# Kernel tuning notes

Measured on AMD Instinct MI355X. Metric: run time of the kernel, lower is better.

## Reference

```python
import jax, jax.numpy as jnp
import numpy as np

IN_CH = 512
STYLE_DIM = 512
K_ATT = 4  # block size used in forward()


def make_up_kernel():
    # make_kernel([1,3,3,1]) -> outer product, normalized; Upsample scales by factor**2
    k = jnp.array([1.0, 3.0, 3.0, 1.0], jnp.float32)
    k = k[None, :] * k[:, None]
    k = k / k.sum()
    return k * 4.0  # factor**2 with factor=2


def setup_inputs() -> dict:
    key = jax.random.key(0)
    ks = jax.random.split(key, 8)
    B, H, W = 8, 128, 128
    return {
        "input": jax.random.normal(ks[0], (B, IN_CH, H, W), jnp.float32),
        "style": jax.random.normal(ks[1], (B, STYLE_DIM), jnp.float32),
        "skip": jax.random.normal(ks[2], (B, 3, H // 2, W // 2), jnp.float32),
        "attention0": jax.random.normal(ks[3], (B, 3, H, W), jnp.float32),
        "attention1": jax.random.normal(ks[4], (B, 3, H, W), jnp.float32),
        # learned params
        "conv_w": jax.random.normal(ks[5], (3, IN_CH), jnp.float32),  # ModulatedConv2d weight (1x1 kernel squeezed)
        "mod_w": jax.random.normal(ks[6], (IN_CH, STYLE_DIM), jnp.float32),  # EqualLinear weight
        "mod_b": jnp.ones((IN_CH,), jnp.float32),  # bias_init=1
        "bias": jnp.zeros((1, 3, 1, 1), jnp.float32),
        "q_w": jax.random.normal(ks[7], (1, 3, 3, 3), jnp.float32) * 0.1,  # query_conv weight [O=1,I=3,3,3]
        "q_b": jnp.zeros((1,), jnp.float32),
        "up_kernel": make_up_kernel(),  # registered buffer
    }


def _upsample2x(x, kernel):
    # upfirdn2d(x, kernel, up=2, pad=(2,1)); kernel is symmetric so flip is a no-op.
    # lhs_dilation=2 inserts zeros between samples (length 2H-1); torch's upfirdn also
    # appends one trailing zero, so the right pad becomes pad1+1 = 2.
    C = x.shape[1]
    k = jnp.broadcast_to(kernel[None, None], (C, 1, 4, 4))
    return jax.lax.conv_general_dilated(
        x, k, window_strides=(1, 1), padding=((2, 2), (2, 2)),
        lhs_dilation=(2, 2), feature_group_count=C)


def _conv3x3(x, w, b):
    out = jax.lax.conv_general_dilated(x, w, (1, 1), ((1, 1), (1, 1)))
    return out + b[None, :, None, None]


def _blockify(x, k):
    # F.unfold(x, k, stride=k) for single-channel x: [B,1,H,W] -> [B, k*k, (H/k)*(W/k)]
    B, _, H, W = x.shape
    x = x.reshape(B, H // k, k, W // k, k)
    return x.transpose(0, 2, 4, 1, 3).reshape(B, k * k, (H // k) * (W // k))


def _unblockify(u, k, H, W):
    # F.fold inverse (non-overlapping): [B, k*k, L] -> [B,1,H,W]
    B = u.shape[0]
    x = u.reshape(B, k, k, H // k, W // k)
    return x.transpose(0, 3, 1, 4, 2).reshape(B, 1, H, W)


def _l2norm(u, axes):
    return u / jnp.maximum(jnp.sqrt(jnp.sum(u * u, axis=axes, keepdims=True)), 1e-12)


def reference(input, style, skip, attention0, attention1,
              conv_w, mod_w, mod_b, bias, q_w, q_b, up_kernel):
    B, Cin, H, W = input.shape
    # EqualLinear modulation: scale = 1/sqrt(style_dim)
    s = style @ (mod_w * (1.0 / np.sqrt(STYLE_DIM))).T + mod_b  # [B, Cin]
    # ModulatedConv2d, kernel_size=1, demodulate=False, group=batch conv -> per-sample scaled 1x1 conv
    conv_scale = 1.0 / np.sqrt(Cin)  # fan_in = in_channel * 1**2
    out = jnp.einsum('oi,bi,bihw->bohw', conv_w * conv_scale, s, input) + bias

    # skip path
    skip_up = _upsample2x(skip, up_kernel)

    # attention map (width > k branch, k=4)
    k = K_ATT
    pq = _conv3x3(jax.lax.stop_gradient(attention0), q_w, q_b)  # [B,1,H,W]
    pk = _conv3x3(jax.lax.stop_gradient(attention1), q_w, q_b)
    qu = _l2norm(_blockify(pq, k), axes=1)  # [B, k*k, L], L2 per column (dim=1)
    ku = _l2norm(_blockify(pk, k), axes=1)
    energy = qu * ku
    energy_star = _l2norm(energy, axes=(1, 2)) * k  # F.normalize over dims (1,2), scaled by k
    att = _unblockify(energy_star, k, H, W)  # [B,1,H,W]

    out = out * att + skip_up * (1.0 - att)
    return out
```

## Files before the change

kernel.cpp:

```cpp
#include <hip/hip_runtime.h>
#include <math.h>

#define HW 16384
#define MOD_BLOCKS 1024

__global__ __launch_bounds__(256) void pre_kernel(
    const float* __restrict__ style, const float* __restrict__ mod_w,
    const float* __restrict__ mod_b, const float* __restrict__ conv_w,
    const float* __restrict__ a0in, const float* __restrict__ a1in,
    const float* __restrict__ q_w, const float* __restrict__ q_b,
    float4* __restrict__ weff4, float* __restrict__ energy,
    float* __restrict__ part) {
  int bid = blockIdx.x;
  int t = threadIdx.x;

  if (bid < MOD_BLOCKS) {
    int wg = bid * 4 + (t >> 6);
    int b = wg >> 9;
    int i = wg & 511;
    int lane = t & 63;
    const float4* row = reinterpret_cast<const float4*>(mod_w + (size_t)i * 512);
    const float4* st = reinterpret_cast<const float4*>(style + (size_t)b * 512);
    float4 r0 = row[lane], r1 = row[lane + 64];
    float4 s0 = st[lane], s1 = st[lane + 64];
    float s = r0.x * s0.x + r0.y * s0.y + r0.z * s0.z + r0.w * s0.w +
              r1.x * s1.x + r1.y * s1.y + r1.z * s1.z + r1.w * s1.w;
#pragma unroll
    for (int m = 1; m < 64; m <<= 1) s += __shfl_xor(s, m);
    if (lane == 0) {
      const float kInv = 0.04419417382415922f;
      s = s * kInv + mod_b[i];
      float4 o;
      o.x = conv_w[i] * kInv * s;
      o.y = conv_w[512 + i] * kInv * s;
      o.z = conv_w[1024 + i] * kInv * s;
      o.w = 0.f;
      weff4[(size_t)b * 512 + i] = o;
    }
    return;
  }

  int blk = bid - MOD_BLOCKS;
  int b = blk >> 6;
  int j = blk & 63;
  int colLocal = t >> 4;
  int pos = t & 15;
  int col = j * 16 + colLocal;
  int by = col >> 5, bx = col & 31;
  int iy = pos >> 2, ix = pos & 3;
  int h = by * 4 + iy, w = bx * 4 + ix;

  __shared__ float qw[27];
  __shared__ float qb;
  if (t < 27) qw[t] = q_w[t];
  if (t == 27) qb = q_b[0];
  __syncthreads();

  float pq = qb, pk = qb;
#pragma unroll
  for (int ci = 0; ci < 3; ++ci) {
    const float* p0 = a0in + (size_t)(b * 3 + ci) * HW;
    const float* p1 = a1in + (size_t)(b * 3 + ci) * HW;
#pragma unroll
    for (int ky = 0; ky < 3; ++ky) {
      int hh = h + ky - 1;
      if ((unsigned)hh >= 128u) continue;
#pragma unroll
      for (int kx = 0; kx < 3; ++kx) {
        int ww = w + kx - 1;
        if ((unsigned)ww >= 128u) continue;
        float wq = qw[ci * 9 + ky * 3 + kx];
        pq = fmaf(wq, p0[hh * 128 + ww], pq);
        pk = fmaf(wq, p1[hh * 128 + ww], pk);
      }
    }
  }
  float sq = pq * pq, sk = pk * pk;
#pragma unroll
  for (int m = 1; m < 16; m <<= 1) {
    sq += __shfl_xor(sq, m);
    sk += __shfl_xor(sk, m);
  }
  float qn = 1.0f / fmaxf(sqrtf(sq), 1e-12f);
  float kn = 1.0f / fmaxf(sqrtf(sk), 1e-12f);
  float e = (pq * qn) * (pk * kn);
  energy[(size_t)b * HW + h * 128 + w] = e;

  float ss = e * e;
#pragma unroll
  for (int m = 1; m < 64; m <<= 1) ss += __shfl_xor(ss, m);
  __shared__ float partl[4];
  int wid = t >> 6;
  if ((t & 63) == 0) partl[wid] = ss;
  __syncthreads();
  if (t == 0) part[blk] = partl[0] + partl[1] + partl[2] + partl[3];
}

__global__ __launch_bounds__(256) void main_kernel(
    const float* __restrict__ input, const float4* __restrict__ weff4,
    const float* __restrict__ bias, const float* __restrict__ skip,
    const float* __restrict__ upk, const float* __restrict__ energy,
    const float* __restrict__ part, float* __restrict__ out) {
  __shared__ float4 lw[512];
  __shared__ float ssq_sh;
  int t = threadIdx.x;
  int blk = blockIdx.x;
  int b = blk >> 6;
  int p = (blk & 63) * 256 + t;

  const float* in = input + (size_t)b * 512 * HW + p;

  float va[32], vb[32];
#pragma unroll
  for (int u = 0; u < 32; ++u) va[u] = in[(size_t)u * HW];

  const float4* g = weff4 + (size_t)b * 512;
  float4 g0 = g[t], g1 = g[t + 256];
  if (t < 64) {
    float ps = part[b * 64 + t];
#pragma unroll
    for (int m = 1; m < 64; m <<= 1) ps += __shfl_xor(ps, m);
    if (t == 0) ssq_sh = ps;
  }
  lw[t] = g0;
  lw[t + 256] = g1;

  float e = energy[(size_t)b * HW + p];
  int y = p >> 7, x = p & 127;
  int syb = ((y + (y & 1)) >> 1) - 1;
  int sxb = ((x + (x & 1)) >> 1) - 1;
  int ky0 = y & 1, kx0 = x & 1;
  float s0 = 0.f, s1 = 0.f, s2 = 0.f;
#pragma unroll
  for (int a = 0; a < 2; ++a) {
    int sy = syb + a;
    if ((unsigned)sy >= 64u) continue;
#pragma unroll
    for (int c2 = 0; c2 < 2; ++c2) {
      int sx = sxb + c2;
      if ((unsigned)sx >= 64u) continue;
      float kv = upk[(ky0 + 2 * a) * 4 + (kx0 + 2 * c2)];
      size_t base = ((size_t)(b * 3) * 64 + sy) * 64 + sx;
      s0 = fmaf(kv, skip[base], s0);
      s1 = fmaf(kv, skip[base + 4096], s1);
      s2 = fmaf(kv, skip[base + 8192], s2);
    }
  }
  float bi0 = bias[0], bi1 = bias[1], bi2 = bias[2];

  __syncthreads();

  float a0 = 0.f, a1 = 0.f, a2 = 0.f;
  for (int c0 = 0; c0 < 512; c0 += 64) {
#pragma unroll
    for (int u = 0; u < 32; ++u) vb[u] = in[(size_t)(c0 + 32 + u) * HW];
#pragma unroll
    for (int u = 0; u < 32; ++u) {
      float4 w = lw[c0 + u];
      a0 = fmaf(w.x, va[u], a0);
      a1 = fmaf(w.y, va[u], a1);
      a2 = fmaf(w.z, va[u], a2);
    }
    if (c0 < 448) {
#pragma unroll
      for (int u = 0; u < 32; ++u) va[u] = in[(size_t)(c0 + 64 + u) * HW];
    }
#pragma unroll
    for (int u = 0; u < 32; ++u) {
      float4 w = lw[c0 + 32 + u];
      a0 = fmaf(w.x, vb[u], a0);
      a1 = fmaf(w.y, vb[u], a1);
      a2 = fmaf(w.z, vb[u], a2);
    }
  }

  float att = e * (4.0f / fmaxf(sqrtf(ssq_sh), 1e-12f));
  float om = 1.0f - att;
  size_t ob = (size_t)(b * 3) * HW + p;
  out[ob] = (a0 + bi0) * att + s0 * om;
  out[ob + HW] = (a1 + bi1) * att + s1 * om;
  out[ob + 2 * HW] = (a2 + bi2) * att + s2 * om;
}

extern "C" void kernel_launch(void* const* d_in, const int* in_sizes, int n_in,
                              void* d_out, int out_size, void* d_ws,
                              size_t ws_size, hipStream_t stream) {
  const float* input  = (const float*)d_in[0];
  const float* style  = (const float*)d_in[1];
  const float* skip   = (const float*)d_in[2];
  const float* att0   = (const float*)d_in[3];
  const float* att1   = (const float*)d_in[4];
  const float* conv_w = (const float*)d_in[5];
  const float* mod_w  = (const float*)d_in[6];
  const float* mod_b  = (const float*)d_in[7];
  const float* bias   = (const float*)d_in[8];
  const float* q_w    = (const float*)d_in[9];
  const float* q_b    = (const float*)d_in[10];
  const float* upk    = (const float*)d_in[11];

  int B = in_sizes[1] / 512;

  float* ws = (float*)d_ws;
  float4* weff4 = (float4*)ws;
  float* energy = ws + 16384;
  float* part   = ws + 16384 + 131072;

  pre_kernel<<<MOD_BLOCKS + B * 64, 256, 0, stream>>>(
      style, mod_w, mod_b, conv_w, att0, att1, q_w, q_b, weff4, energy, part);
  main_kernel<<<B * 64, 256, 0, stream>>>(input, weff4, bias, skip, upk,
                                          energy, part, (float*)d_out);
}
```

Measured before the change: 58.64 us.

## Split channel reduction across waves with float4 pixel loads and LDS combine

Measured after the change: 60.01 us. 2.3% more time.

```diff
diff --git a/kernel.cpp b/kernel.cpp
--- a/kernel.cpp
+++ b/kernel.cpp
@@ -2,6 +2,7 @@
 #include <math.h>
 
 #define HW 16384
+#define PX4 4096
 #define MOD_BLOCKS 1024
 
 __global__ __launch_bounds__(256) void pre_kernel(
@@ -102,17 +103,14 @@
     const float* __restrict__ upk, const float* __restrict__ energy,
     const float* __restrict__ part, float* __restrict__ out) {
   __shared__ float4 lw[512];
+  __shared__ float lds_part[4 * 64 * 13];
   __shared__ float ssq_sh;
   int t = threadIdx.x;
   int blk = blockIdx.x;
   int b = blk >> 6;
-  int p = (blk & 63) * 256 + t;
-
-  const float* in = input + (size_t)b * 512 * HW + p;
-
-  float va[32], vb[32];
-#pragma unroll
-  for (int u = 0; u < 32; ++u) va[u] = in[(size_t)u * HW];
+  int j = blk & 63;
+  int s = t & 63;
+  int w = t >> 6;
 
   const float4* g = weff4 + (size_t)b * 512;
   float4 g0 = g[t], g1 = g[t + 256];
@@ -125,12 +123,13 @@
   lw[t] = g0;
   lw[t + 256] = g1;
 
+  int p = j * 256 + t;
   float e = energy[(size_t)b * HW + p];
   int y = p >> 7, x = p & 127;
   int syb = ((y + (y & 1)) >> 1) - 1;
   int sxb = ((x + (x & 1)) >> 1) - 1;
   int ky0 = y & 1, kx0 = x & 1;
-  float s0 = 0.f, s1 = 0.f, s2 = 0.f;
+  float sk0 = 0.f, sk1 = 0.f, sk2 = 0.f;
 #pragma unroll
   for (int a = 0; a < 2; ++a) {
     int sy = syb + a;
@@ -141,45 +140,68 @@
       if ((unsigned)sx >= 64u) continue;
       float kv = upk[(ky0 + 2 * a) * 4 + (kx0 + 2 * c2)];
       size_t base = ((size_t)(b * 3) * 64 + sy) * 64 + sx;
-      s0 = fmaf(kv, skip[base], s0);
-      s1 = fmaf(kv, skip[base + 4096], s1);
-      s2 = fmaf(kv, skip[base + 8192], s2);
+      sk0 = fmaf(kv, skip[base], sk0);
+      sk1 = fmaf(kv, skip[base + 4096], sk1);
+      sk2 = fmaf(kv, skip[base + 8192], sk2);
     }
   }
   float bi0 = bias[0], bi1 = bias[1], bi2 = bias[2];
 
   __syncthreads();
 
+  const float4* in4 = reinterpret_cast<const float4*>(input) +
+                      ((size_t)b * 512 + w * 128) * PX4 + (size_t)j * 64 + s;
+  float A0[4] = {0.f, 0.f, 0.f, 0.f};
+  float A1[4] = {0.f, 0.f, 0.f, 0.f};
+  float A2[4] = {0.f, 0.f, 0.f, 0.f};
+  int cbase = w * 128;
+  for (int c0 = 0; c0 < 128; c0 += 16) {
+    float4 v[16];
+#pragma unroll
+    for (int u = 0; u < 16; ++u) v[u] = in4[(size_t)(c0 + u) * PX4];
+#pragma unroll
+    for (int u = 0; u < 16; ++u) {
+      float4 wv = lw[cbase + c0 + u];
+      A0[0] = fmaf(wv.x, v[u].x, A0[0]);
+      A0[1] = fmaf(wv.x, v[u].y, A0[1]);
+      A0[2] = fmaf(wv.x, v[u].z, A0[2]);
+      A0[3] = fmaf(wv.x, v[u].w, A0[3]);
+      A1[0] = fmaf(wv.y, v[u].x, A1[0]);
+      A1[1] = fmaf(wv.y, v[u].y, A1[1]);
+      A1[2] = fmaf(wv.y, v[u].z, A1[2]);
+      A1[3] = fmaf(wv.y, v[u].w, A1[3]);
+      A2[0] = fmaf(wv.z, v[u].x, A2[0]);
+      A2[1] = fmaf(wv.z, v[u].y, A2[1]);
+      A2[2] = fmaf(wv.z, v[u].z, A2[2]);
+      A2[3] = fmaf(wv.z, v[u].w, A2[3]);
+    }
+  }
+
+  float* mp = &lds_part[(w * 64 + s) * 13];
+#pragma unroll
+  for (int i = 0; i < 4; ++i) {
+    mp[i] = A0[i];
+    mp[4 + i] = A1[i];
+    mp[8 + i] = A2[i];
+  }
+  __syncthreads();
+
+  int slot = t >> 2, sub = t & 3;
   float a0 = 0.f, a1 = 0.f, a2 = 0.f;
-  for (int c0 = 0; c0 < 512; c0 += 64) {
-#pragma unroll
-    for (int u = 0; u < 32; ++u) vb[u] = in[(size_t)(c0 + 32 + u) * HW];
-#pragma unroll
-    for (int u = 0; u < 32; ++u) {
-      float4 w = lw[c0 + u];
-      a0 = fmaf(w.x, va[u], a0);
-      a1 = fmaf(w.y, va[u], a1);
-      a2 = fmaf(w.z, va[u], a2);
-    }
-    if (c0 < 448) {
-#pragma unroll
-      for (int u = 0; u < 32; ++u) va[u] = in[(size_t)(c0 + 64 + u) * HW];
-    }
-#pragma unroll
-    for (int u = 0; u < 32; ++u) {
-      float4 w = lw[c0 + 32 + u];
-      a0 = fmaf(w.x, vb[u], a0);
-      a1 = fmaf(w.y, vb[u], a1);
-      a2 = fmaf(w.z, vb[u], a2);
-    }
+#pragma unroll
+  for (int ww = 0; ww < 4; ++ww) {
+    const float* q = &lds_part[(ww * 64 + slot) * 13];
+    a0 += q[sub];
+    a1 += q[4 + sub];
+    a2 += q[8 + sub];
   }
 
   float att = e * (4.0f / fmaxf(sqrtf(ssq_sh), 1e-12f));
   float om = 1.0f - att;
   size_t ob = (size_t)(b * 3) * HW + p;
-  out[ob] = (a0 + bi0) * att + s0 * om;
-  out[ob + HW] = (a1 + bi1) * att + s1 * om;
-  out[ob + 2 * HW] = (a2 + bi2) * att + s2 * om;
+  out[ob] = (a0 + bi0) * att + sk0 * om;
+  out[ob + HW] = (a1 + bi1) * att + sk1 * om;
+  out[ob + 2 * HW] = (a2 + bi2) * att + sk2 * om;
 }
 
 extern "C" void kernel_launch(void* const* d_in, const int* in_sizes, int n_in,
```

## Restructure style modulation to reuse mod_w rows across batch and simplify main loop

Applied to the files above, without the earlier changes.

New measurement: 60.18 us. +2.6%, slower.

```diff
diff --git a/kernel.cpp b/kernel.cpp
--- a/kernel.cpp
+++ b/kernel.cpp
@@ -2,7 +2,7 @@
 #include <math.h>
 
 #define HW 16384
-#define MOD_BLOCKS 1024
+#define MOD_BLOCKS 64
 
 __global__ __launch_bounds__(256) void pre_kernel(
     const float* __restrict__ style, const float* __restrict__ mod_w,
@@ -13,29 +13,38 @@
     float* __restrict__ part) {
   int bid = blockIdx.x;
   int t = threadIdx.x;
+  const float kInv = 0.04419417382415922f;
 
   if (bid < MOD_BLOCKS) {
-    int wg = bid * 4 + (t >> 6);
-    int b = wg >> 9;
-    int i = wg & 511;
-    int lane = t & 63;
-    const float4* row = reinterpret_cast<const float4*>(mod_w + (size_t)i * 512);
-    const float4* st = reinterpret_cast<const float4*>(style + (size_t)b * 512);
-    float4 r0 = row[lane], r1 = row[lane + 64];
-    float4 s0 = st[lane], s1 = st[lane + 64];
-    float s = r0.x * s0.x + r0.y * s0.y + r0.z * s0.z + r0.w * s0.w +
-              r1.x * s1.x + r1.y * s1.y + r1.z * s1.z + r1.w * s1.w;
-#pragma unroll
-    for (int m = 1; m < 64; m <<= 1) s += __shfl_xor(s, m);
-    if (lane == 0) {
-      const float kInv = 0.04419417382415922f;
-      s = s * kInv + mod_b[i];
-      float4 o;
-      o.x = conv_w[i] * kInv * s;
-      o.y = conv_w[512 + i] * kInv * s;
-      o.z = conv_w[1024 + i] * kInv * s;
-      o.w = 0.f;
-      weff4[(size_t)b * 512 + i] = o;
+    __shared__ float4 st4[1024];
+    const float4* sg = reinterpret_cast<const float4*>(style);
+#pragma unroll
+    for (int k = 0; k < 4; ++k) st4[t + k * 256] = sg[t + k * 256];
+    __syncthreads();
+
+    int cl = t >> 5;
+    int rem = t & 31;
+    int b = rem >> 2;
+    int q = rem & 3;
+    int c = bid * 8 + cl;
+
+    const float4* row = reinterpret_cast<const float4*>(mod_w + (size_t)c * 512)
+                        + q * 32;
+    const float4* sv = st4 + b * 128 + q * 32;
+    float s = 0.f;
+#pragma unroll
+    for (int u = 0; u < 32; ++u) {
+      float4 r = row[u];
+      float4 sx = sv[u];
+      s += r.x * sx.x + r.y * sx.y + r.z * sx.z + r.w * sx.w;
+    }
+    s += __shfl_xor(s, 1);
+    s += __shfl_xor(s, 2);
+    if (q == 0) {
+      float sm = s * kInv + mod_b[c];
+      weff4[(size_t)b * 512 + c] =
+          make_float4(conv_w[c] * kInv * sm, conv_w[512 + c] * kInv * sm,
+                      conv_w[1024 + c] * kInv * sm, 0.f);
     }
     return;
   }
@@ -52,6 +61,7 @@
 
   __shared__ float qw[27];
   __shared__ float qb;
+  __shared__ float partl[4];
   if (t < 27) qw[t] = q_w[t];
   if (t == 27) qb = q_b[0];
   __syncthreads();
@@ -89,7 +99,6 @@
   float ss = e * e;
 #pragma unroll
   for (int m = 1; m < 64; m <<= 1) ss += __shfl_xor(ss, m);
-  __shared__ float partl[4];
   int wid = t >> 6;
   if ((t & 63) == 0) partl[wid] = ss;
   __syncthreads();
@@ -110,7 +119,7 @@
 
   const float* in = input + (size_t)b * 512 * HW + p;
 
-  float va[32], vb[32];
+  float va[32];
 #pragma unroll
   for (int u = 0; u < 32; ++u) va[u] = in[(size_t)u * HW];
 
@@ -151,26 +160,24 @@
   __syncthreads();
 
   float a0 = 0.f, a1 = 0.f, a2 = 0.f;
-  for (int c0 = 0; c0 < 512; c0 += 64) {
-#pragma unroll
-    for (int u = 0; u < 32; ++u) vb[u] = in[(size_t)(c0 + 32 + u) * HW];
+#pragma unroll
+  for (int u = 0; u < 32; ++u) {
+    float4 w = lw[u];
+    a0 = fmaf(w.x, va[u], a0);
+    a1 = fmaf(w.y, va[u], a1);
+    a2 = fmaf(w.z, va[u], a2);
+  }
+
+  for (int c0 = 32; c0 < 512; c0 += 32) {
+    float v[32];
+#pragma unroll
+    for (int u = 0; u < 32; ++u) v[u] = in[(size_t)(c0 + u) * HW];
 #pragma unroll
     for (int u = 0; u < 32; ++u) {
       float4 w = lw[c0 + u];
-      a0 = fmaf(w.x, va[u], a0);
-      a1 = fmaf(w.y, va[u], a1);
-      a2 = fmaf(w.z, va[u], a2);
-    }
-    if (c0 < 448) {
-#pragma unroll
-      for (int u = 0; u < 32; ++u) va[u] = in[(size_t)(c0 + 64 + u) * HW];
-    }
-#pragma unroll
-    for (int u = 0; u < 32; ++u) {
-      float4 w = lw[c0 + 32 + u];
-      a0 = fmaf(w.x, vb[u], a0);
-      a1 = fmaf(w.y, vb[u], a1);
-      a2 = fmaf(w.z, vb[u], a2);
+      a0 = fmaf(w.x, v[u], a0);
+      a1 = fmaf(w.y, v[u], a1);
+      a2 = fmaf(w.z, v[u], a2);
     }
   }
 
```
